# Optimization experiments

Hardware: AMD Instinct MI355X
Metric: run time of the kernel (lower is better)

## Reference

```python
import jax, jax.numpy as jnp
import numpy as np

U, I, E, D, R = 100000, 50000, 2000000, 64, 5


def setup_inputs() -> dict:
    key = jax.random.key(0)
    ks = jax.random.split(key, 14)
    def n(k, shape, scale=0.05):
        return jax.random.normal(k, shape, jnp.float32) * scale
    return {
        "user_feat": n(ks[0], (U, D), 1.0),
        "item_feat": n(ks[1], (I, D), 1.0),
        "rating_feat": n(ks[2], (R, D), 1.0),
        "row_idxs": jax.random.randint(ks[3], (E,), 0, I),   # item index per edge
        "col_idxs": jax.random.randint(ks[4], (E,), 0, U),   # user index per edge (dst)
        "rating": jax.random.randint(ks[5], (E,), 0, R),
        # gv = Linear(2D,D)+ReLU -> Linear(D,D)+ReLU
        "gv_w1": n(ks[6], (2 * D, D)), "gv_b1": jnp.zeros((D,), jnp.float32),
        "gv_w2": n(ks[7], (D, D)),     "gv_b2": jnp.zeros((D,), jnp.float32),
        # Attention: Linear(2D,D)+ReLU -> Linear(D,D)+ReLU -> Linear(D,1)
        "att_w1": n(ks[8], (2 * D, D)), "att_b1": jnp.zeros((D,), jnp.float32),
        "att_w2": n(ks[9], (D, D)),     "att_b2": jnp.zeros((D,), jnp.float32),
        "att_w3": n(ks[10], (D, 1)),    "att_b3": jnp.zeros((1,), jnp.float32),
        # output projection w = Linear(D,D)
        "w_w": n(ks[11], (D, D)), "w_b": jnp.zeros((D,), jnp.float32),
    }


def segment_softmax(logits, seg, num_segments):
    # numerically stable softmax over edges grouped by destination node
    m = jax.ops.segment_max(logits, seg, num_segments=num_segments)
    e = jnp.exp(logits - m[seg])
    s = jax.ops.segment_sum(e, seg, num_segments=num_segments)
    return e / s[seg]


def reference(user_feat, item_feat, rating_feat, row_idxs, col_idxs, rating,
              gv_w1, gv_b1, gv_w2, gv_b2,
              att_w1, att_b1, att_w2, att_b2, att_w3, att_b3,
              w_w, w_b):
    # gather per-edge embeddings
    r_emb = rating_feat[rating]          # [E, D]
    i_emb = item_feat[row_idxs]          # [E, D]
    u_emb = user_feat[col_idxs]          # [E, D]
    # gv MLP on concat(item, rating)
    x = jnp.concatenate([i_emb, r_emb], axis=1)              # [E, 2D]
    h1 = jax.nn.relu(x @ gv_w1 + gv_b1)
    x_ia = jax.nn.relu(h1 @ gv_w2 + gv_b2)                   # [E, D]
    # attention MLP on concat(x_ia, user)
    a = jnp.concatenate([x_ia, u_emb], axis=1)               # [E, 2D]
    a = jax.nn.relu(a @ att_w1 + att_b1)
    a = jax.nn.relu(a @ att_w2 + att_b2)
    weight = (a @ att_w3 + att_b3)[:, 0]                     # [E]
    # edge_softmax over incoming edges of each destination (user) node
    value = segment_softmax(weight, col_idxs, U)             # [E]
    # scatter-sum weighted messages to users
    h = jax.ops.segment_sum(x_ia * value[:, None], col_idxs, num_segments=U)  # [U, D]
    # act is None -> plain linear
    return h @ w_w + w_b
```

## Files before the change

### kernel.cpp

```cpp
#include <hip/hip_runtime.h>
#include <hip/hip_bf16.h>
#include <hip/hip_fp8.h>

#define U_N 100000
#define I_N 50000
#define E_N 2000000
#define R_N 5
#define C_N (I_N*R_N)
#define NBLK_E 7813
#define NBLK_C 1954
#define NBUCKC 196

typedef __hip_bfloat16 bf16_t;
typedef unsigned short u16;
typedef unsigned char u8;
typedef __attribute__((ext_vector_type(8))) short bf16x8;
typedef __attribute__((ext_vector_type(4))) float f32x4;

__device__ __forceinline__ float blo(unsigned u){ return __uint_as_float(u<<16); }
__device__ __forceinline__ float bhi(unsigned u){ return __uint_as_float(u & 0xffff0000u); }
__device__ __forceinline__ unsigned pkbf(float a, float b){
  __hip_bfloat162 t = __float22bfloat162_rn(float2{a,b});
  union { __hip_bfloat162 h; unsigned u; } cv; cv.h = t; return cv.u;
}
__device__ __forceinline__ u16 f2b(float v){
  union { __hip_bfloat16 h; u16 u; } cv; cv.h = __float2bfloat16(v); return cv.u;
}
__device__ __forceinline__ unsigned ff8(float f){
  __hip_fp8_e4m3 h(f); return (unsigned)h.__x;
}
__device__ __forceinline__ float2 f8x2(u16 h){
  __hip_fp8x2_e4m3 v; v.__x = h; return (float2)v;
}

__global__ __launch_bounds__(256) void k_histQ(const int* __restrict__ cols, int* __restrict__ hist_g){
  __shared__ int histI[NBUCKC];
  int t = threadIdx.x, b = blockIdx.x;
  if(t < NBUCKC) histI[t] = 0;
  __syncthreads();
  int e = b*256 + t;
  if(e < E_N) atomicAdd(&histI[cols[e] >> 9], 1);
  __syncthreads();
  if(t < NBUCKC) hist_g[(size_t)b*NBUCKC + t] = histI[t];
}

__global__ __launch_bounds__(256) void k_scanQ(const int* __restrict__ hist_g, int* __restrict__ boff_g,
                                               int* __restrict__ qtot){
  __shared__ int wsum[4];
  int t = threadIdx.x, q = blockIdx.x;
  int lane = t & 63, wv = t >> 6;
  int running = 0;
  for(int c0=0; c0<NBLK_E; c0+=256){
    int b = c0 + t;
    int v = (b < NBLK_E) ? hist_g[(size_t)b*NBUCKC + q] : 0;
    int inc = v;
#pragma unroll
    for(int off=1; off<64; off<<=1){
      int x = __shfl(inc, lane-off);
      if(lane >= off) inc += x;
    }
    if(lane == 63) wsum[wv] = inc;
    __syncthreads();
    int w0=wsum[0], w1=wsum[1], w2=wsum[2], w3=wsum[3];
    int wpre = (wv>0?w0:0) + (wv>1?w1:0) + (wv>2?w2:0);
    if(b < NBLK_E) boff_g[(size_t)b*NBUCKC + q] = running + wpre + inc - v;
    running += w0 + w1 + w2 + w3;
    __syncthreads();
  }
  if(t == 0) qtot[q] = running;
}

__global__ void k_scanT(const int* __restrict__ qtot, int* __restrict__ qbase){
  __shared__ int s[256];
  int t = threadIdx.x;
  int v = (t < NBUCKC) ? qtot[t] : 0;
  s[t] = v; __syncthreads();
  for(int off=1; off<256; off<<=1){
    int x = (t>=off) ? s[t-off] : 0;
    __syncthreads();
    s[t] += x;
    __syncthreads();
  }
  if(t < NBUCKC) qbase[t] = s[t] - v;
  if(t == 255)   qbase[NBUCKC] = s[255];
}

__global__ __launch_bounds__(256) void k_blockq(const int* __restrict__ qbase, int* __restrict__ blockq){
  int b = blockIdx.x*256 + threadIdx.x; if(b >= NBLK_E) return;
  int e = b*256;
  int lo = 0, hi = NBUCKC-1;
  while(lo < hi){ int mid = (lo+hi+1)>>1; if(qbase[mid] <= e) lo = mid; else hi = mid-1; }
  blockq[b] = lo;
}

__global__ __launch_bounds__(256) void k_place2(const int* __restrict__ rows, const int* __restrict__ cols,
                                                const int* __restrict__ rats,
                                                const int* __restrict__ boff_g, const int* __restrict__ qbase,
                                                unsigned* __restrict__ uc2){
  __shared__ int rankI[NBUCKC];
  __shared__ int baseI[NBUCKC];
  int t = threadIdx.x, b = blockIdx.x;
  if(t < NBUCKC){
    rankI[t] = 0;
    baseI[t] = qbase[t] + boff_g[(size_t)b*NBUCKC + t];
  }
  __syncthreads();
  int e = b*256 + t;
  if(e < E_N){
    int u = cols[e];
    int c = rows[e]*5 + rats[e];
    int q = u >> 9;
    int r = atomicAdd(&rankI[q], 1);
    uc2[baseI[q] + r] = ((unsigned)(u & 16383) << 18) | (unsigned)c;
  }
}

__global__ __launch_bounds__(256) void k_fine(const unsigned* __restrict__ uc2, const int* __restrict__ qbase,
                                              unsigned* __restrict__ uc3, int* __restrict__ start){
  __shared__ int histv[512];
  __shared__ int s[512];
  __shared__ int fillb[512];
  int t = threadIdx.x, q = blockIdx.x;
  histv[t]=0; histv[t+256]=0; fillb[t]=0; fillb[t+256]=0;
  __syncthreads();
  int r0 = qbase[q], r1 = qbase[q+1];
  for(int j=r0+t; j<r1; j+=256) atomicAdd(&histv[(uc2[j]>>18)&511], 1);
  __syncthreads();
  s[t]=histv[t]; s[t+256]=histv[t+256];
  __syncthreads();
  for(int off=1; off<512; off<<=1){
    int a0 = (t>=off)? s[t-off] : 0;
    int a1 = (t+256>=off)? s[t+256-off] : 0;
    __syncthreads();
    s[t]+=a0; s[t+256]+=a1;
    __syncthreads();
  }
  int e0 = s[t]-histv[t], e1 = s[t+256]-histv[t+256];
  start[q*512+t]     = r0 + e0;
  start[q*512+t+256] = r0 + e1;
  s[t]=e0; s[t+256]=e1;
  __syncthreads();
  for(int j=r0+t; j<r1; j+=256){
    unsigned v = uc2[j];
    int ul = (int)((v>>18)&511);
    int off = atomicAdd(&fillb[ul], 1);
    uc3[r0 + s[ul] + off] = v;
  }
}

__global__ void k_ratpart(const float* __restrict__ rf, const float* __restrict__ w1,
                          const float* __restrict__ b1, float* __restrict__ out){
  int t = threadIdx.x; if(t >= R_N*64) return;
  int r = t>>6, d = t&63;
  float acc = b1[d];
  for(int k=0;k<64;k++) acc += rf[r*64 + k] * w1[(64+k)*64 + d];
  out[t] = acc;
}

__global__ __launch_bounds__(256) void k_prepw6(const float* __restrict__ w1, const float* __restrict__ a1,
                                                const float* __restrict__ w2, const float* __restrict__ a2,
                                                const float* __restrict__ ww,
                                                u16* w1t, u16* u1t, u16* w2t, u16* a1t, u16* a2t, u16* wwt){
  int idx = (blockIdx.x & 15)*256 + threadIdx.x;
  int sec = blockIdx.x >> 4;
  int d = idx >> 6, k = idx & 63;
  const float* src; u16* dst; int ko = 0;
  switch(sec){
    case 0: src=w1; dst=w1t; break;
    case 1: src=a1; dst=u1t; ko=64; break;
    case 2: src=w2; dst=w2t; break;
    case 3: src=a1; dst=a1t; break;
    case 4: src=a2; dst=a2t; break;
    default: src=ww; dst=wwt; break;
  }
  dst[idx] = f2b(src[(size_t)(ko+k)*64 + d]);
}

template<bool BIAS>
__global__ __launch_bounds__(256) void k_rowgemm(const float4* __restrict__ in,
                                                 const uint4* __restrict__ wt,
                                                 const float* __restrict__ bias,
                                                 uint4* __restrict__ outp, int n){
  __shared__ uint4 A_u4[2048];
  __shared__ uint4 W_u4[512];
  __shared__ float bsh[64];
  u16* A16 = (u16*)A_u4;
  const int tid = threadIdx.x;
  for(int cid = tid; cid < 512; cid += 256){
    int dd = cid >> 3, ch = cid & 7;
    W_u4[dd*8 + (ch ^ (dd&7))] = wt[cid];
  }
  if(BIAS && tid < 64) bsh[tid] = bias[tid];
  const int base = blockIdx.x*256;
  const int ch = tid & 7;
#pragma unroll
  for(int it=0; it<8; ++it){
    int s = it*32 + (tid>>3);
    int r = base + s;
    uint4 o = {0,0,0,0};
    if(r < n){
      const float4* p = in + (size_t)r*16 + ch*2;
      float4 v0 = p[0], v1 = p[1];
      o.x = pkbf(v0.x, v0.y); o.y = pkbf(v0.z, v0.w);
      o.z = pkbf(v1.x, v1.y); o.w = pkbf(v1.z, v1.w);
    }
    A_u4[s*8 + (ch ^ (s&7))] = o;
  }
  __syncthreads();
  const int l = tid & 63, w = tid >> 6;
  const int lr = l & 15, g = l >> 4;
  bf16x8 bfr[4][2];
#pragma unroll
  for(int nt=0; nt<4; ++nt)
#pragma unroll
    for(int kk=0; kk<2; ++kk){
      int d = nt*16 + lr;
      bfr[nt][kk] = *(const bf16x8*)&W_u4[d*8 + ((kk*4+g) ^ (d&7))];
    }
  float bv[4];
#pragma unroll
  for(int nt=0; nt<4; ++nt) bv[nt] = BIAS ? bsh[nt*16 + lr] : 0.f;
#pragma unroll
  for(int t=0; t<4; ++t){
    int s = w*64 + t*16 + lr;
    bf16x8 af0 = *(const bf16x8*)&A_u4[s*8 + ((0*4+g) ^ (s&7))];
    bf16x8 af1 = *(const bf16x8*)&A_u4[s*8 + ((1*4+g) ^ (s&7))];
    f32x4 acc[4];
#pragma unroll
    for(int nt=0; nt<4; ++nt){
      f32x4 c0 = { bv[nt], bv[nt], bv[nt], bv[nt] };
      c0 = __builtin_amdgcn_mfma_f32_16x16x32_bf16(af0, bfr[nt][0], c0, 0, 0, 0);
      c0 = __builtin_amdgcn_mfma_f32_16x16x32_bf16(af1, bfr[nt][1], c0, 0, 0, 0);
      acc[nt] = c0;
    }
#pragma unroll
    for(int nt=0; nt<4; ++nt){
      int d = nt*16 + lr;
#pragma unroll
      for(int reg=0; reg<4; ++reg){
        int srow = w*64 + t*16 + g*4 + reg;
        A16[srow*64 + ((d>>3)^(srow&7))*8 + (d&7)] = f2b(acc[nt][reg]);
      }
    }
  }
#pragma unroll
  for(int it=0; it<8; ++it){
    int s = w*64 + it*8 + (l>>3);
    int c2 = l & 7;
    int r = base + s;
    if(r < n) outp[(size_t)r*8 + c2] = A_u4[s*8 + (c2 ^ (s&7))];
  }
}

__global__ __launch_bounds__(256) void k_combo_mfma(const uint4* __restrict__ itemp,
                                                    const float4* __restrict__ ratp,
                                                    const uint4* __restrict__ w2t_g, const uint4* __restrict__ a1t_g,
                                                    const uint4* __restrict__ wwt_g,
                                                    const float* __restrict__ b2,
                                                    uint4* __restrict__ y_o, u8* __restrict__ xa1_o8){
  __shared__ uint4 A_u4[1024];
  __shared__ uint4 X_u4[1024];
  __shared__ uint4 W2_u4[512];
  __shared__ uint4 A1_u4[512];
  __shared__ uint4 WW_u4[512];
  __shared__ float4 rsh4[80];
  __shared__ float b2sh[64];
  u16* A16 = (u16*)A_u4;
  u16* X16 = (u16*)X_u4;
  const int tid = threadIdx.x;
  for(int cid = tid; cid < 512; cid += 256){
    int dd = cid >> 3, ch = cid & 7;
    W2_u4[dd*8 + (ch ^ (dd&7))] = w2t_g[cid];
    A1_u4[dd*8 + (ch ^ (dd&7))] = a1t_g[cid];
    WW_u4[dd*8 + (ch ^ (dd&7))] = wwt_g[cid];
  }
  if(tid < 80) rsh4[tid] = ratp[tid];
  if(tid < 64) b2sh[tid] = b2[tid];
  __syncthreads();

  const int base = blockIdx.x*128;
  const int ch = tid & 7;
#pragma unroll
  for(int it=0; it<4; ++it){
    int s = it*32 + (tid>>3);
    int cidx = base + s;
    uint4 o = {0,0,0,0};
    if(cidx < C_N){
      int i = cidx/5, r = cidx - i*5;
      uint4 iv = itemp[(size_t)i*8 + ch];
      float4 r0 = rsh4[r*16 + ch*2], r1 = rsh4[r*16 + ch*2 + 1];
      o.x = pkbf(fmaxf(blo(iv.x)+r0.x,0.f), fmaxf(bhi(iv.x)+r0.y,0.f));
      o.y = pkbf(fmaxf(blo(iv.y)+r0.z,0.f), fmaxf(bhi(iv.y)+r0.w,0.f));
      o.z = pkbf(fmaxf(blo(iv.z)+r1.x,0.f), fmaxf(bhi(iv.z)+r1.y,0.f));
      o.w = pkbf(fmaxf(blo(iv.w)+r1.z,0.f), fmaxf(bhi(iv.w)+r1.w,0.f));
    }
    A_u4[s*8 + (ch ^ (s&7))] = o;
  }
  __syncthreads();

  const int l = tid & 63, w = tid >> 6;
  const int lr = l & 15, g = l >> 4;
  bf16x8 w2f[4][2], a1f[4][2], wwf[4][2];
#pragma unroll
  for(int nt=0; nt<4; ++nt)
#pragma unroll
    for(int kk=0; kk<2; ++kk){
      int d = nt*16 + lr;
      w2f[nt][kk] = *(const bf16x8*)&W2_u4[d*8 + ((kk*4+g) ^ (d&7))];
      a1f[nt][kk] = *(const bf16x8*)&A1_u4[d*8 + ((kk*4+g) ^ (d&7))];
      wwf[nt][kk] = *(const bf16x8*)&WW_u4[d*8 + ((kk*4+g) ^ (d&7))];
    }
  float b2v[4];
#pragma unroll
  for(int nt=0; nt<4; ++nt) b2v[nt] = b2sh[nt*16 + lr];

#pragma unroll
  for(int t=0; t<2; ++t){
    int s = w*32 + t*16 + lr;
    bf16x8 af0 = *(const bf16x8*)&A_u4[s*8 + ((0*4+g) ^ (s&7))];
    bf16x8 af1 = *(const bf16x8*)&A_u4[s*8 + ((1*4+g) ^ (s&7))];
#pragma unroll
    for(int nt=0; nt<4; ++nt){
      f32x4 c0 = { b2v[nt], b2v[nt], b2v[nt], b2v[nt] };
      c0 = __builtin_amdgcn_mfma_f32_16x16x32_bf16(af0, w2f[nt][0], c0, 0, 0, 0);
      c0 = __builtin_amdgcn_mfma_f32_16x16x32_bf16(af1, w2f[nt][1], c0, 0, 0, 0);
      int d = nt*16 + lr;
#pragma unroll
      for(int reg=0; reg<4; ++reg){
        int srow = w*32 + t*16 + g*4 + reg;
        X16[srow*64 + ((d>>3)^(srow&7))*8 + (d&7)] = f2b(fmaxf(c0[reg], 0.f));
      }
    }
    bf16x8 xf0 = *(const bf16x8*)&X_u4[s*8 + ((0*4+g) ^ (s&7))];
    bf16x8 xf1 = *(const bf16x8*)&X_u4[s*8 + ((1*4+g) ^ (s&7))];
#pragma unroll
    for(int nt=0; nt<4; ++nt){
      f32x4 c0 = { 0.f, 0.f, 0.f, 0.f };
      c0 = __builtin_amdgcn_mfma_f32_16x16x32_bf16(xf0, a1f[nt][0], c0, 0, 0, 0);
      c0 = __builtin_amdgcn_mfma_f32_16x16x32_bf16(xf1, a1f[nt][1], c0, 0, 0, 0);
      int d = nt*16 + lr;
#pragma unroll
      for(int reg=0; reg<4; ++reg){
        int srow = w*32 + t*16 + g*4 + reg;
        A16[srow*64 + ((d>>3)^(srow&7))*8 + (d&7)] = f2b(c0[reg]);
      }
    }
#pragma unroll
    for(int nt=0; nt<4; ++nt){
      f32x4 c0 = { 0.f, 0.f, 0.f, 0.f };
      c0 = __builtin_amdgcn_mfma_f32_16x16x32_bf16(xf0, wwf[nt][0], c0, 0, 0, 0);
      c0 = __builtin_amdgcn_mfma_f32_16x16x32_bf16(xf1, wwf[nt][1], c0, 0, 0, 0);
      int d = nt*16 + lr;
#pragma unroll
      for(int reg=0; reg<4; ++reg){
        int srow = w*32 + t*16 + g*4 + reg;
        X16[srow*64 + ((d>>3)^(srow&7))*8 + (d&7)] = f2b(c0[reg]);
      }
    }
  }
#pragma unroll
  for(int it=0; it<4; ++it){
    int s = w*32 + it*8 + (l>>3);
    int c2 = l & 7;
    int r = base + s;
    if(r < C_N) y_o[(size_t)r*8 + c2] = X_u4[s*8 + (c2 ^ (s&7))];
  }
#pragma unroll
  for(int it=0; it<2; ++it){
    int slot = it*64 + l;
    int rl = slot >> 2;
    int c4 = slot & 3;
    int s = w*32 + rl;
    int r = base + s;
    if(r < C_N){
      uint4 h0 = A_u4[s*8 + ((c4*2+0) ^ (s&7))];
      uint4 h1 = A_u4[s*8 + ((c4*2+1) ^ (s&7))];
      uint4 o;
      o.x = ff8(blo(h0.x)) | (ff8(bhi(h0.x))<<8) | (ff8(blo(h0.y))<<16) | (ff8(bhi(h0.y))<<24);
      o.y = ff8(blo(h0.z)) | (ff8(bhi(h0.z))<<8) | (ff8(blo(h0.w))<<16) | (ff8(bhi(h0.w))<<24);
      o.z = ff8(blo(h1.x)) | (ff8(bhi(h1.x))<<8) | (ff8(blo(h1.y))<<16) | (ff8(bhi(h1.y))<<24);
      o.w = ff8(blo(h1.z)) | (ff8(bhi(h1.z))<<8) | (ff8(blo(h1.w))<<16) | (ff8(bhi(h1.w))<<24);
      *(uint4*)(xa1_o8 + (size_t)r*64 + c4*16) = o;
    }
  }
}

__global__ __launch_bounds__(256) void k_edge_mfma(const unsigned* __restrict__ uc3,
                                                   const int* __restrict__ qbase, const int* __restrict__ blockq,
                                                   const u8* __restrict__ xa1p8, const uint4* __restrict__ userp,
                                                   const u16* __restrict__ w2t_g,
                                                   const float* __restrict__ a2b,
                                                   const float* __restrict__ a3w, const float* __restrict__ a3b,
                                                   float* __restrict__ wlog){
  const int tid = threadIdx.x;
  const int base = blockIdx.x*256;
  const int l = tid & 63, w = tid >> 6;
  const int lr = l & 15;
  const int g  = l >> 4;
  bf16x8 bf[4][2];
#pragma unroll
  for(int nt=0; nt<4; ++nt)
#pragma unroll
    for(int kk=0; kk<2; ++kk){
      int d = nt*16 + lr;
      bf[nt][kk] = *(const bf16x8*)(w2t_g + d*64 + kk*32 + g*8);
    }
  float b2v[4], a3v[4];
#pragma unroll
  for(int nt=0; nt<4; ++nt){ b2v[nt] = a2b[nt*16 + lr]; a3v[nt] = a3w[nt*16 + lr]; }
  const float a3b0 = a3b[0];

  int cin[4], uin[4];
  int bq = blockq[blockIdx.x];
#pragma unroll
  for(int t=0; t<4; ++t){
    int s = base + w*64 + t*16 + lr;
    int sc = (s < E_N) ? s : (E_N-1);
    unsigned vv = (s < E_N) ? uc3[s] : 0u;
    int q = bq;
    while(sc >= qbase[q+1]) ++q;
    cin[t] = (int)(vv & 0x3FFFFu);
    uin[t] = (q<<9) | (int)((vv>>18) & 511u);
  }

  auto compute = [&](uint2 xq0, uint2 xq1, uint4 uv0, uint4 uv1, int t){
    union { uint4 u4; bf16x8 v; } a0, a1;
    {
      float2 p01 = f8x2((u16)xq0.x), p23 = f8x2((u16)(xq0.x>>16));
      float2 p45 = f8x2((u16)xq0.y), p67 = f8x2((u16)(xq0.y>>16));
      a0.u4.x = pkbf(fmaxf(p01.x+blo(uv0.x),0.f), fmaxf(p01.y+bhi(uv0.x),0.f));
      a0.u4.y = pkbf(fmaxf(p23.x+blo(uv0.y),0.f), fmaxf(p23.y+bhi(uv0.y),0.f));
      a0.u4.z = pkbf(fmaxf(p45.x+blo(uv0.z),0.f), fmaxf(p45.y+bhi(uv0.z),0.f));
      a0.u4.w = pkbf(fmaxf(p67.x+blo(uv0.w),0.f), fmaxf(p67.y+bhi(uv0.w),0.f));
      p01 = f8x2((u16)xq1.x); p23 = f8x2((u16)(xq1.x>>16));
      p45 = f8x2((u16)xq1.y); p67 = f8x2((u16)(xq1.y>>16));
      a1.u4.x = pkbf(fmaxf(p01.x+blo(uv1.x),0.f), fmaxf(p01.y+bhi(uv1.x),0.f));
      a1.u4.y = pkbf(fmaxf(p23.x+blo(uv1.y),0.f), fmaxf(p23.y+bhi(uv1.y),0.f));
      a1.u4.z = pkbf(fmaxf(p45.x+blo(uv1.z),0.f), fmaxf(p45.y+bhi(uv1.z),0.f));
      a1.u4.w = pkbf(fmaxf(p67.x+blo(uv1.w),0.f), fmaxf(p67.y+bhi(uv1.w),0.f));
    }
    f32x4 acc[4];
#pragma unroll
    for(int nt=0; nt<4; ++nt){
      f32x4 c0 = { b2v[nt], b2v[nt], b2v[nt], b2v[nt] };
      c0 = __builtin_amdgcn_mfma_f32_16x16x32_bf16(a0.v, bf[nt][0], c0, 0, 0, 0);
      c0 = __builtin_amdgcn_mfma_f32_16x16x32_bf16(a1.v, bf[nt][1], c0, 0, 0, 0);
      acc[nt] = c0;
    }
    float s0=0.f, s1=0.f, s2=0.f, s3=0.f;
#pragma unroll
    for(int nt=0; nt<4; ++nt){
      s0 += fmaxf(acc[nt][0], 0.f) * a3v[nt];
      s1 += fmaxf(acc[nt][1], 0.f) * a3v[nt];
      s2 += fmaxf(acc[nt][2], 0.f) * a3v[nt];
      s3 += fmaxf(acc[nt][3], 0.f) * a3v[nt];
    }
#pragma unroll
    for(int mask=1; mask<16; mask<<=1){
      s0 += __shfl_xor(s0, mask);
      s1 += __shfl_xor(s1, mask);
      s2 += __shfl_xor(s2, mask);
      s3 += __shfl_xor(s3, mask);
    }
    if(lr == 0){
      int e0 = base + w*64 + t*16 + g*4;
      if(e0+0 < E_N) wlog[e0+0] = s0 + a3b0;
      if(e0+1 < E_N) wlog[e0+1] = s1 + a3b0;
      if(e0+2 < E_N) wlog[e0+2] = s2 + a3b0;
      if(e0+3 < E_N) wlog[e0+3] = s3 + a3b0;
    }
  };

  uint2 xA0 = *(const uint2*)(xa1p8 + (size_t)cin[0]*64 + g*8);
  uint2 xA1 = *(const uint2*)(xa1p8 + (size_t)cin[0]*64 + 32 + g*8);
  uint4 uA0 = userp[(size_t)uin[0]*8 + g];
  uint4 uA1 = userp[(size_t)uin[0]*8 + 4 + g];
  uint2 xB0 = *(const uint2*)(xa1p8 + (size_t)cin[1]*64 + g*8);
  uint2 xB1 = *(const uint2*)(xa1p8 + (size_t)cin[1]*64 + 32 + g*8);
  uint4 uB0 = userp[(size_t)uin[1]*8 + g];
  uint4 uB1 = userp[(size_t)uin[1]*8 + 4 + g];

  compute(xA0, xA1, uA0, uA1, 0);
  xA0 = *(const uint2*)(xa1p8 + (size_t)cin[2]*64 + g*8);
  xA1 = *(const uint2*)(xa1p8 + (size_t)cin[2]*64 + 32 + g*8);
  uA0 = userp[(size_t)uin[2]*8 + g];
  uA1 = userp[(size_t)uin[2]*8 + 4 + g];
  compute(xB0, xB1, uB0, uB1, 1);
  xB0 = *(const uint2*)(xa1p8 + (size_t)cin[3]*64 + g*8);
  xB1 = *(const uint2*)(xa1p8 + (size_t)cin[3]*64 + 32 + g*8);
  uB0 = userp[(size_t)uin[3]*8 + g];
  uB1 = userp[(size_t)uin[3]*8 + 4 + g];
  compute(xA0, xA1, uA0, uA1, 2);
  compute(xB0, xB1, uB0, uB1, 3);
}

__global__ __launch_bounds__(256) void k_aggf(const int* __restrict__ start,
                                              const unsigned* __restrict__ uc3,
                                              const float* __restrict__ wlog,
                                              const u16* __restrict__ Y,
                                              const float* __restrict__ wb,
                                              float* __restrict__ out){
  __shared__ uint4 Ysh[2][4][256];
  int w = threadIdx.x >> 6, l = threadIdx.x & 63;
  int lr = l & 15, g = l >> 4;
  int base = (blockIdx.x*4 + w) * 16;
  if(base >= U_N) return;
  int s0g = start[base];
  int s1g = start[base+16];
  unsigned ml = (unsigned)((base + lr) & 16383);
  int sA = s0g & ~31;
  int nch = (s1g - sA + 31) >> 5;
  const int kb = g*8;

  f32x4 acc[4];
#pragma unroll
  for(int nt=0; nt<4; ++nt) acc[nt] = f32x4{0.f,0.f,0.f,0.f};
  float ssum = 0.f;
  int buf = 0;
  if(nch > 0){
    int rowe = sA + (l>>1);
    int crow = (int)(uc3[rowe] & 0x3FFFFu);
    const uint4* yp = (const uint4*)Y + (size_t)crow*8 + (l&1)*4;
    uint4 y0=yp[0], y1=yp[1], y2=yp[2], y3=yp[3];
    uint4* dst = &Ysh[0][w][(l>>1)*8 + (l&1)*4];
    dst[0]=y0; dst[1]=y1; dst[2]=y2; dst[3]=y3;
  }
  for(int ch=0; ch<nch; ++ch){
    int e0 = sA + ch*32;
    uint4 n0, n1, n2, n3;
    bool hasNext = (ch+1 < nch);
    if(hasNext){
      int rowe = e0 + 32 + (l>>1);
      int crowN = (int)(uc3[rowe] & 0x3FFFFu);
      const uint4* yp = (const uint4*)Y + (size_t)crowN*8 + (l&1)*4;
      n0=yp[0]; n1=yp[1]; n2=yp[2]; n3=yp[3];
    }
    float4 wv0 = *(const float4*)(wlog + e0 + kb);
    float4 wv1 = *(const float4*)(wlog + e0 + kb + 4);
    uint4 v0 = *(const uint4*)(uc3 + e0 + kb);
    uint4 v1 = *(const uint4*)(uc3 + e0 + kb + 4);
    bf16x8 af;
    {
      bool mt; float e;
      mt = ((v0.x>>18)==ml); e = __expf(mt?wv0.x:-1e30f); ssum += e; af[0] = mt?(short)f2b(e):(short)0;
      mt = ((v0.y>>18)==ml); e = __expf(mt?wv0.y:-1e30f); ssum += e; af[1] = mt?(short)f2b(e):(short)0;
      mt = ((v0.z>>18)==ml); e = __expf(mt?wv0.z:-1e30f); ssum += e; af[2] = mt?(short)f2b(e):(short)0;
      mt = ((v0.w>>18)==ml); e = __expf(mt?wv0.w:-1e30f); ssum += e; af[3] = mt?(short)f2b(e):(short)0;
      mt = ((v1.x>>18)==ml); e = __expf(mt?wv1.x:-1e30f); ssum += e; af[4] = mt?(short)f2b(e):(short)0;
      mt = ((v1.y>>18)==ml); e = __expf(mt?wv1.y:-1e30f); ssum += e; af[5] = mt?(short)f2b(e):(short)0;
      mt = ((v1.z>>18)==ml); e = __expf(mt?wv1.z:-1e30f); ssum += e; af[6] = mt?(short)f2b(e):(short)0;
      mt = ((v1.w>>18)==ml); e = __expf(mt?wv1.w:-1e30f); ssum += e; af[7] = mt?(short)f2b(e):(short)0;
    }
    u16* Ysh16 = (u16*)&Ysh[buf][w][0];
    bf16x8 b0, b1, b2, b3;
#pragma unroll
    for(int j=0; j<8; ++j){
      int r = (kb + j)*64 + lr;
      b0[j] = (short)Ysh16[r];
      b1[j] = (short)Ysh16[r+16];
      b2[j] = (short)Ysh16[r+32];
      b3[j] = (short)Ysh16[r+48];
    }
    acc[0] = __builtin_amdgcn_mfma_f32_16x16x32_bf16(af, b0, acc[0], 0, 0, 0);
    acc[1] = __builtin_amdgcn_mfma_f32_16x16x32_bf16(af, b1, acc[1], 0, 0, 0);
    acc[2] = __builtin_amdgcn_mfma_f32_16x16x32_bf16(af, b2, acc[2], 0, 0, 0);
    acc[3] = __builtin_amdgcn_mfma_f32_16x16x32_bf16(af, b3, acc[3], 0, 0, 0);
    if(hasNext){
      uint4* dst = &Ysh[buf^1][w][(l>>1)*8 + (l&1)*4];
      dst[0]=n0; dst[1]=n1; dst[2]=n2; dst[3]=n3;
    }
    buf ^= 1;
  }
  ssum += __shfl_xor(ssum, 16);
  ssum += __shfl_xor(ssum, 32);
  float inv = (ssum > 0.f) ? (1.f/ssum) : 0.f;
  float wbv[4];
#pragma unroll
  for(int nt=0; nt<4; ++nt) wbv[nt] = wb[nt*16 + lr];
#pragma unroll
  for(int reg=0; reg<4; ++reg){
    float sc = __shfl(inv, g*4 + reg);
    int u = base + g*4 + reg;
#pragma unroll
    for(int nt=0; nt<4; ++nt)
      out[(size_t)u*64 + nt*16 + lr] = acc[nt][reg]*sc + wbv[nt];
  }
}

extern "C" void kernel_launch(void* const* d_in, const int* in_sizes, int n_in,
                              void* d_out, int out_size, void* d_ws, size_t ws_size,
                              hipStream_t stream){
  (void)in_sizes; (void)n_in; (void)out_size; (void)ws_size;
  const float4* user_feat  = (const float4*)d_in[0];
  const float4* item_feat  = (const float4*)d_in[1];
  const float*  rating_feat= (const float*)d_in[2];
  const int*    rows       = (const int*)d_in[3];
  const int*    cols       = (const int*)d_in[4];
  const int*    rats       = (const int*)d_in[5];
  const float* gv_w1 = (const float*)d_in[6];
  const float* gv_b1 = (const float*)d_in[7];
  const float* gv_w2 = (const float*)d_in[8];
  const float* gv_b2 = (const float*)d_in[9];
  const float* att_w1= (const float*)d_in[10];
  const float* att_b1= (const float*)d_in[11];
  const float* att_w2= (const float*)d_in[12];
  const float* att_b2= (const float*)d_in[13];
  const float* att_w3= (const float*)d_in[14];
  const float* att_b3= (const float*)d_in[15];
  const float* w_w   = (const float*)d_in[16];
  const float* w_b   = (const float*)d_in[17];
  float* out = (float*)d_out;

  char* ws = (char*)d_ws; size_t off = 0;
  auto take = [&](size_t b)->char*{ char* p = ws + off; off = (off + b + 255) & ~(size_t)255; return p; };
  bf16_t*   item_part  = (bf16_t*)take((size_t)I_N*64*2);
  bf16_t*   user_part  = (bf16_t*)take((size_t)U_N*64*2);
  float*    rating_part= (float*) take((size_t)R_N*64*4);
  bf16_t*   y_t        = (bf16_t*)take((size_t)C_N*64*2);
  u8*       xa1_8      = (u8*)    take((size_t)C_N*64);
  float*    wlog_s     = (float*) take((size_t)E_N*4);
  unsigned* uc3        = (unsigned*)take((size_t)E_N*4);
  unsigned* uc2        = (unsigned*)take((size_t)E_N*4);
  int*      hist_g     = (int*)   take((size_t)NBLK_E*NBUCKC*4);
  int*      boff_g     = (int*)   take((size_t)NBLK_E*NBUCKC*4);
  int*      qtot       = (int*)   take((size_t)256*4);
  int*      qbase      = (int*)   take((size_t)256*4);
  int*      blockq     = (int*)   take((size_t)NBLK_E*4);
  int*      start      = (int*)   take((size_t)(NBUCKC*512+64)*4);
  u16*      w1t        = (u16*)   take((size_t)4096*2);
  u16*      u1t        = (u16*)   take((size_t)4096*2);
  u16*      w2t        = (u16*)   take((size_t)4096*2);
  u16*      a1t        = (u16*)   take((size_t)4096*2);
  u16*      a2t        = (u16*)   take((size_t)4096*2);
  u16*      wwt        = (u16*)   take((size_t)4096*2);

  k_histQ <<<NBLK_E, 256, 0, stream>>>(cols, hist_g);
  k_scanQ <<<NBUCKC, 256, 0, stream>>>(hist_g, boff_g, qtot);
  k_scanT <<<1, 256, 0, stream>>>(qtot, qbase);
  k_blockq<<<(NBLK_E+255)/256, 256, 0, stream>>>(qbase, blockq);
  k_place2<<<NBLK_E, 256, 0, stream>>>(rows, cols, rats, boff_g, qbase, uc2);
  k_fine  <<<NBUCKC, 256, 0, stream>>>(uc2, qbase, uc3, start);
  k_ratpart <<<1, 320, 0, stream>>>(rating_feat, gv_w1, gv_b1, rating_part);
  k_prepw6  <<<96, 256, 0, stream>>>(gv_w1, att_w1, gv_w2, att_w2, w_w, w1t, u1t, w2t, a1t, a2t, wwt);
  k_rowgemm<false><<<(I_N+255)/256, 256, 0, stream>>>(item_feat, (const uint4*)w1t, nullptr,
                                                      (uint4*)item_part, I_N);
  k_rowgemm<true> <<<(U_N+255)/256, 256, 0, stream>>>(user_feat, (const uint4*)u1t, att_b1,
                                                      (uint4*)user_part, U_N);
  k_combo_mfma<<<NBLK_C, 256, 0, stream>>>((const uint4*)item_part, (const float4*)rating_part,
                                           (const uint4*)w2t, (const uint4*)a1t, (const uint4*)wwt, gv_b2,
                                           (uint4*)y_t, xa1_8);
  k_edge_mfma<<<NBLK_E, 256, 0, stream>>>(uc3, qbase, blockq, xa1_8, (const uint4*)user_part,
                                          w2t, att_b2, att_w3, att_b3, wlog_s);
  k_aggf <<<(U_N/64)+1, 256, 0, stream>>>(start, uc3, wlog_s, (const u16*)y_t, w_b, out);
}
```

Before: 263.8 us.

## Fuse edge attention MLP into per-user aggregation kernel

Merges the per-edge attention MLP kernel and the aggregation kernel into one kernel that works per group of 16 destination users. Each wave computes attention logits for its 32-edge chunk, exponentiates them into shared memory and uses them directly as softmax weights. The user rows come from a shared-memory tile, so the wlog buffer round trip, the blockq kernel and the per-edge user gathers all go away. In exchange, edges in chunks that straddle user-group boundaries are computed more than once, the Y double-buffer prefetch is removed, and the max subtraction is dropped from the softmax (it was already absent before).

Measured after the change: 277.8 us. 5.3% more time.

```diff
diff --git a/kernel.cpp b/kernel.cpp
--- a/kernel.cpp
+++ b/kernel.cpp
@@ -83,14 +83,6 @@
   }
   if(t < NBUCKC) qbase[t] = s[t] - v;
   if(t == 255)   qbase[NBUCKC] = s[255];
-}
-
-__global__ __launch_bounds__(256) void k_blockq(const int* __restrict__ qbase, int* __restrict__ blockq){
-  int b = blockIdx.x*256 + threadIdx.x; if(b >= NBLK_E) return;
-  int e = b*256;
-  int lo = 0, hi = NBUCKC-1;
-  while(lo < hi){ int mid = (lo+hi+1)>>1; if(qbase[mid] <= e) lo = mid; else hi = mid-1; }
-  blockq[b] = lo;
 }
 
 __global__ __launch_bounds__(256) void k_place2(const int* __restrict__ rows, const int* __restrict__ cols,
@@ -385,18 +377,25 @@
   }
 }
 
-__global__ __launch_bounds__(256) void k_edge_mfma(const unsigned* __restrict__ uc3,
-                                                   const int* __restrict__ qbase, const int* __restrict__ blockq,
-                                                   const u8* __restrict__ xa1p8, const uint4* __restrict__ userp,
-                                                   const u16* __restrict__ w2t_g,
-                                                   const float* __restrict__ a2b,
-                                                   const float* __restrict__ a3w, const float* __restrict__ a3b,
-                                                   float* __restrict__ wlog){
+__global__ __launch_bounds__(256) void k_fused(const int* __restrict__ start,
+                                               const unsigned* __restrict__ uc3,
+                                               const u8* __restrict__ xa1p8,
+                                               const uint4* __restrict__ userp,
+                                               const u16* __restrict__ w2t_g,
+                                               const float* __restrict__ a2b,
+                                               const float* __restrict__ a3w, const float* __restrict__ a3b,
+                                               const u16* __restrict__ Y,
+                                               const float* __restrict__ wb,
+                                               float* __restrict__ out){
+  __shared__ uint4 Ush[4][16][8];
+  __shared__ uint4 Ysh[4][256];
+  __shared__ float pl[4][32];
   const int tid = threadIdx.x;
-  const int base = blockIdx.x*256;
-  const int l = tid & 63, w = tid >> 6;
-  const int lr = l & 15;
-  const int g  = l >> 4;
+  int w = tid >> 6, l = tid & 63;
+  int lr = l & 15, g = l >> 4;
+  int base = (blockIdx.x*4 + w) * 16;
+  if(base >= U_N) return;
+
   bf16x8 bf[4][2];
 #pragma unroll
   for(int nt=0; nt<4; ++nt)
@@ -410,104 +409,15 @@
   for(int nt=0; nt<4; ++nt){ b2v[nt] = a2b[nt*16 + lr]; a3v[nt] = a3w[nt*16 + lr]; }
   const float a3b0 = a3b[0];
 
-  int cin[4], uin[4];
-  int bq = blockq[blockIdx.x];
-#pragma unroll
-  for(int t=0; t<4; ++t){
-    int s = base + w*64 + t*16 + lr;
-    int sc = (s < E_N) ? s : (E_N-1);
-    unsigned vv = (s < E_N) ? uc3[s] : 0u;
-    int q = bq;
-    while(sc >= qbase[q+1]) ++q;
-    cin[t] = (int)(vv & 0x3FFFFu);
-    uin[t] = (q<<9) | (int)((vv>>18) & 511u);
-  }
-
-  auto compute = [&](uint2 xq0, uint2 xq1, uint4 uv0, uint4 uv1, int t){
-    union { uint4 u4; bf16x8 v; } a0, a1;
-    {
-      float2 p01 = f8x2((u16)xq0.x), p23 = f8x2((u16)(xq0.x>>16));
-      float2 p45 = f8x2((u16)xq0.y), p67 = f8x2((u16)(xq0.y>>16));
-      a0.u4.x = pkbf(fmaxf(p01.x+blo(uv0.x),0.f), fmaxf(p01.y+bhi(uv0.x),0.f));
-      a0.u4.y = pkbf(fmaxf(p23.x+blo(uv0.y),0.f), fmaxf(p23.y+bhi(uv0.y),0.f));
-      a0.u4.z = pkbf(fmaxf(p45.x+blo(uv0.z),0.f), fmaxf(p45.y+bhi(uv0.z),0.f));
-      a0.u4.w = pkbf(fmaxf(p67.x+blo(uv0.w),0.f), fmaxf(p67.y+bhi(uv0.w),0.f));
-      p01 = f8x2((u16)xq1.x); p23 = f8x2((u16)(xq1.x>>16));
-      p45 = f8x2((u16)xq1.y); p67 = f8x2((u16)(xq1.y>>16));
-      a1.u4.x = pkbf(fmaxf(p01.x+blo(uv1.x),0.f), fmaxf(p01.y+bhi(uv1.x),0.f));
-      a1.u4.y = pkbf(fmaxf(p23.x+blo(uv1.y),0.f), fmaxf(p23.y+bhi(uv1.y),0.f));
-      a1.u4.z = pkbf(fmaxf(p45.x+blo(uv1.z),0.f), fmaxf(p45.y+bhi(uv1.z),0.f));
-      a1.u4.w = pkbf(fmaxf(p67.x+blo(uv1.w),0.f), fmaxf(p67.y+bhi(uv1.w),0.f));
-    }
-    f32x4 acc[4];
-#pragma unroll
-    for(int nt=0; nt<4; ++nt){
-      f32x4 c0 = { b2v[nt], b2v[nt], b2v[nt], b2v[nt] };
-      c0 = __builtin_amdgcn_mfma_f32_16x16x32_bf16(a0.v, bf[nt][0], c0, 0, 0, 0);
-      c0 = __builtin_amdgcn_mfma_f32_16x16x32_bf16(a1.v, bf[nt][1], c0, 0, 0, 0);
-      acc[nt] = c0;
-    }
-    float s0=0.f, s1=0.f, s2=0.f, s3=0.f;
-#pragma unroll
-    for(int nt=0; nt<4; ++nt){
-      s0 += fmaxf(acc[nt][0], 0.f) * a3v[nt];
-      s1 += fmaxf(acc[nt][1], 0.f) * a3v[nt];
-      s2 += fmaxf(acc[nt][2], 0.f) * a3v[nt];
-      s3 += fmaxf(acc[nt][3], 0.f) * a3v[nt];
-    }
-#pragma unroll
-    for(int mask=1; mask<16; mask<<=1){
-      s0 += __shfl_xor(s0, mask);
-      s1 += __shfl_xor(s1, mask);
-      s2 += __shfl_xor(s2, mask);
-      s3 += __shfl_xor(s3, mask);
-    }
-    if(lr == 0){
-      int e0 = base + w*64 + t*16 + g*4;
-      if(e0+0 < E_N) wlog[e0+0] = s0 + a3b0;
-      if(e0+1 < E_N) wlog[e0+1] = s1 + a3b0;
-      if(e0+2 < E_N) wlog[e0+2] = s2 + a3b0;
-      if(e0+3 < E_N) wlog[e0+3] = s3 + a3b0;
-    }
-  };
-
-  uint2 xA0 = *(const uint2*)(xa1p8 + (size_t)cin[0]*64 + g*8);
-  uint2 xA1 = *(const uint2*)(xa1p8 + (size_t)cin[0]*64 + 32 + g*8);
-  uint4 uA0 = userp[(size_t)uin[0]*8 + g];
-  uint4 uA1 = userp[(size_t)uin[0]*8 + 4 + g];
-  uint2 xB0 = *(const uint2*)(xa1p8 + (size_t)cin[1]*64 + g*8);
-  uint2 xB1 = *(const uint2*)(xa1p8 + (size_t)cin[1]*64 + 32 + g*8);
-  uint4 uB0 = userp[(size_t)uin[1]*8 + g];
-  uint4 uB1 = userp[(size_t)uin[1]*8 + 4 + g];
-
-  compute(xA0, xA1, uA0, uA1, 0);
-  xA0 = *(const uint2*)(xa1p8 + (size_t)cin[2]*64 + g*8);
-  xA1 = *(const uint2*)(xa1p8 + (size_t)cin[2]*64 + 32 + g*8);
-  uA0 = userp[(size_t)uin[2]*8 + g];
-  uA1 = userp[(size_t)uin[2]*8 + 4 + g];
-  compute(xB0, xB1, uB0, uB1, 1);
-  xB0 = *(const uint2*)(xa1p8 + (size_t)cin[3]*64 + g*8);
-  xB1 = *(const uint2*)(xa1p8 + (size_t)cin[3]*64 + 32 + g*8);
-  uB0 = userp[(size_t)uin[3]*8 + g];
-  uB1 = userp[(size_t)uin[3]*8 + 4 + g];
-  compute(xA0, xA1, uA0, uA1, 2);
-  compute(xB0, xB1, uB0, uB1, 3);
-}
-
-__global__ __launch_bounds__(256) void k_aggf(const int* __restrict__ start,
-                                              const unsigned* __restrict__ uc3,
-                                              const float* __restrict__ wlog,
-                                              const u16* __restrict__ Y,
-                                              const float* __restrict__ wb,
-                                              float* __restrict__ out){
-  __shared__ uint4 Ysh[2][4][256];
-  int w = threadIdx.x >> 6, l = threadIdx.x & 63;
-  int lr = l & 15, g = l >> 4;
-  int base = (blockIdx.x*4 + w) * 16;
-  if(base >= U_N) return;
+  {
+    int idx0 = l*2;
+    int row = idx0 >> 3, col = idx0 & 7;
+    Ush[w][row][col]   = userp[(size_t)(base+row)*8 + col];
+    Ush[w][row][col+1] = userp[(size_t)(base+row)*8 + col+1];
+  }
+
   int s0g = start[base];
   int s1g = start[base+16];
-  unsigned ml = (unsigned)((base + lr) & 16383);
   int sA = s0g & ~31;
   int nch = (s1g - sA + 31) >> 5;
   const int kb = g*8;
@@ -516,42 +426,89 @@
 #pragma unroll
   for(int nt=0; nt<4; ++nt) acc[nt] = f32x4{0.f,0.f,0.f,0.f};
   float ssum = 0.f;
-  int buf = 0;
-  if(nch > 0){
-    int rowe = sA + (l>>1);
+
+  for(int ch=0; ch<nch; ++ch){
+    int e0 = sA + ch*32;
+    int rowe = e0 + (l>>1);
     int crow = (int)(uc3[rowe] & 0x3FFFFu);
     const uint4* yp = (const uint4*)Y + (size_t)crow*8 + (l&1)*4;
     uint4 y0=yp[0], y1=yp[1], y2=yp[2], y3=yp[3];
-    uint4* dst = &Ysh[0][w][(l>>1)*8 + (l&1)*4];
-    dst[0]=y0; dst[1]=y1; dst[2]=y2; dst[3]=y3;
-  }
-  for(int ch=0; ch<nch; ++ch){
-    int e0 = sA + ch*32;
-    uint4 n0, n1, n2, n3;
-    bool hasNext = (ch+1 < nch);
-    if(hasNext){
-      int rowe = e0 + 32 + (l>>1);
-      int crowN = (int)(uc3[rowe] & 0x3FFFFu);
-      const uint4* yp = (const uint4*)Y + (size_t)crowN*8 + (l&1)*4;
-      n0=yp[0]; n1=yp[1]; n2=yp[2]; n3=yp[3];
-    }
-    float4 wv0 = *(const float4*)(wlog + e0 + kb);
-    float4 wv1 = *(const float4*)(wlog + e0 + kb + 4);
+
+#pragma unroll
+    for(int t=0; t<2; ++t){
+      int et = e0 + t*16 + lr;
+      unsigned v = uc3[et];
+      int c = (int)(v & 0x3FFFFu);
+      unsigned ul = ((v>>18) - (unsigned)base) & 16383u;
+      int ulc = (ul < 16u) ? (int)ul : 0;
+      uint2 xq0 = *(const uint2*)(xa1p8 + (size_t)c*64 + g*8);
+      uint2 xq1 = *(const uint2*)(xa1p8 + (size_t)c*64 + 32 + g*8);
+      uint4 uv0 = Ush[w][ulc][g];
+      uint4 uv1 = Ush[w][ulc][4+g];
+      union { uint4 u4; bf16x8 v8; } a0, a1;
+      {
+        float2 p01 = f8x2((u16)xq0.x), p23 = f8x2((u16)(xq0.x>>16));
+        float2 p45 = f8x2((u16)xq0.y), p67 = f8x2((u16)(xq0.y>>16));
+        a0.u4.x = pkbf(fmaxf(p01.x+blo(uv0.x),0.f), fmaxf(p01.y+bhi(uv0.x),0.f));
+        a0.u4.y = pkbf(fmaxf(p23.x+blo(uv0.y),0.f), fmaxf(p23.y+bhi(uv0.y),0.f));
+        a0.u4.z = pkbf(fmaxf(p45.x+blo(uv0.z),0.f), fmaxf(p45.y+bhi(uv0.z),0.f));
+        a0.u4.w = pkbf(fmaxf(p67.x+blo(uv0.w),0.f), fmaxf(p67.y+bhi(uv0.w),0.f));
+        p01 = f8x2((u16)xq1.x); p23 = f8x2((u16)(xq1.x>>16));
+        p45 = f8x2((u16)xq1.y); p67 = f8x2((u16)(xq1.y>>16));
+        a1.u4.x = pkbf(fmaxf(p01.x+blo(uv1.x),0.f), fmaxf(p01.y+bhi(uv1.x),0.f));
+        a1.u4.y = pkbf(fmaxf(p23.x+blo(uv1.y),0.f), fmaxf(p23.y+bhi(uv1.y),0.f));
+        a1.u4.z = pkbf(fmaxf(p45.x+blo(uv1.z),0.f), fmaxf(p45.y+bhi(uv1.z),0.f));
+        a1.u4.w = pkbf(fmaxf(p67.x+blo(uv1.w),0.f), fmaxf(p67.y+bhi(uv1.w),0.f));
+      }
+      f32x4 acc2[4];
+#pragma unroll
+      for(int nt=0; nt<4; ++nt){
+        f32x4 c0 = { b2v[nt], b2v[nt], b2v[nt], b2v[nt] };
+        c0 = __builtin_amdgcn_mfma_f32_16x16x32_bf16(a0.v8, bf[nt][0], c0, 0, 0, 0);
+        c0 = __builtin_amdgcn_mfma_f32_16x16x32_bf16(a1.v8, bf[nt][1], c0, 0, 0, 0);
+        acc2[nt] = c0;
+      }
+      float s0=0.f, s1=0.f, s2=0.f, s3=0.f;
+#pragma unroll
+      for(int nt=0; nt<4; ++nt){
+        s0 += fmaxf(acc2[nt][0], 0.f) * a3v[nt];
+        s1 += fmaxf(acc2[nt][1], 0.f) * a3v[nt];
+        s2 += fmaxf(acc2[nt][2], 0.f) * a3v[nt];
+        s3 += fmaxf(acc2[nt][3], 0.f) * a3v[nt];
+      }
+#pragma unroll
+      for(int mask=1; mask<16; mask<<=1){
+        s0 += __shfl_xor(s0, mask);
+        s1 += __shfl_xor(s1, mask);
+        s2 += __shfl_xor(s2, mask);
+        s3 += __shfl_xor(s3, mask);
+      }
+      if(lr == 0){
+        pl[w][t*16 + g*4 + 0] = __expf(s0 + a3b0);
+        pl[w][t*16 + g*4 + 1] = __expf(s1 + a3b0);
+        pl[w][t*16 + g*4 + 2] = __expf(s2 + a3b0);
+        pl[w][t*16 + g*4 + 3] = __expf(s3 + a3b0);
+      }
+    }
+    {
+      uint4* dst = &Ysh[w][(l>>1)*8 + (l&1)*4];
+      dst[0]=y0; dst[1]=y1; dst[2]=y2; dst[3]=y3;
+    }
     uint4 v0 = *(const uint4*)(uc3 + e0 + kb);
     uint4 v1 = *(const uint4*)(uc3 + e0 + kb + 4);
     bf16x8 af;
     {
-      bool mt; float e;
-      mt = ((v0.x>>18)==ml); e = __expf(mt?wv0.x:-1e30f); ssum += e; af[0] = mt?(short)f2b(e):(short)0;
-      mt = ((v0.y>>18)==ml); e = __expf(mt?wv0.y:-1e30f); ssum += e; af[1] = mt?(short)f2b(e):(short)0;
-      mt = ((v0.z>>18)==ml); e = __expf(mt?wv0.z:-1e30f); ssum += e; af[2] = mt?(short)f2b(e):(short)0;
-      mt = ((v0.w>>18)==ml); e = __expf(mt?wv0.w:-1e30f); ssum += e; af[3] = mt?(short)f2b(e):(short)0;
-      mt = ((v1.x>>18)==ml); e = __expf(mt?wv1.x:-1e30f); ssum += e; af[4] = mt?(short)f2b(e):(short)0;
-      mt = ((v1.y>>18)==ml); e = __expf(mt?wv1.y:-1e30f); ssum += e; af[5] = mt?(short)f2b(e):(short)0;
-      mt = ((v1.z>>18)==ml); e = __expf(mt?wv1.z:-1e30f); ssum += e; af[6] = mt?(short)f2b(e):(short)0;
-      mt = ((v1.w>>18)==ml); e = __expf(mt?wv1.w:-1e30f); ssum += e; af[7] = mt?(short)f2b(e):(short)0;
-    }
-    u16* Ysh16 = (u16*)&Ysh[buf][w][0];
+      float pv; bool mt;
+      mt = ((((v0.x>>18) - (unsigned)base) & 16383u) == (unsigned)lr); pv = pl[w][kb+0]; ssum += mt?pv:0.f; af[0] = mt?(short)f2b(pv):(short)0;
+      mt = ((((v0.y>>18) - (unsigned)base) & 16383u) == (unsigned)lr); pv = pl[w][kb+1]; ssum += mt?pv:0.f; af[1] = mt?(short)f2b(pv):(short)0;
+      mt = ((((v0.z>>18) - (unsigned)base) & 16383u) == (unsigned)lr); pv = pl[w][kb+2]; ssum += mt?pv:0.f; af[2] = mt?(short)f2b(pv):(short)0;
+      mt = ((((v0.w>>18) - (unsigned)base) & 16383u) == (unsigned)lr); pv = pl[w][kb+3]; ssum += mt?pv:0.f; af[3] = mt?(short)f2b(pv):(short)0;
+      mt = ((((v1.x>>18) - (unsigned)base) & 16383u) == (unsigned)lr); pv = pl[w][kb+4]; ssum += mt?pv:0.f; af[4] = mt?(short)f2b(pv):(short)0;
+      mt = ((((v1.y>>18) - (unsigned)base) & 16383u) == (unsigned)lr); pv = pl[w][kb+5]; ssum += mt?pv:0.f; af[5] = mt?(short)f2b(pv):(short)0;
+      mt = ((((v1.z>>18) - (unsigned)base) & 16383u) == (unsigned)lr); pv = pl[w][kb+6]; ssum += mt?pv:0.f; af[6] = mt?(short)f2b(pv):(short)0;
+      mt = ((((v1.w>>18) - (unsigned)base) & 16383u) == (unsigned)lr); pv = pl[w][kb+7]; ssum += mt?pv:0.f; af[7] = mt?(short)f2b(pv):(short)0;
+    }
+    u16* Ysh16 = (u16*)&Ysh[w][0];
     bf16x8 b0, b1, b2, b3;
 #pragma unroll
     for(int j=0; j<8; ++j){
@@ -565,11 +522,6 @@
     acc[1] = __builtin_amdgcn_mfma_f32_16x16x32_bf16(af, b1, acc[1], 0, 0, 0);
     acc[2] = __builtin_amdgcn_mfma_f32_16x16x32_bf16(af, b2, acc[2], 0, 0, 0);
     acc[3] = __builtin_amdgcn_mfma_f32_16x16x32_bf16(af, b3, acc[3], 0, 0, 0);
-    if(hasNext){
-      uint4* dst = &Ysh[buf^1][w][(l>>1)*8 + (l&1)*4];
-      dst[0]=n0; dst[1]=n1; dst[2]=n2; dst[3]=n3;
-    }
-    buf ^= 1;
   }
   ssum += __shfl_xor(ssum, 16);
   ssum += __shfl_xor(ssum, 32);
@@ -618,14 +570,12 @@
   float*    rating_part= (float*) take((size_t)R_N*64*4);
   bf16_t*   y_t        = (bf16_t*)take((size_t)C_N*64*2);
   u8*       xa1_8      = (u8*)    take((size_t)C_N*64);
-  float*    wlog_s     = (float*) take((size_t)E_N*4);
   unsigned* uc3        = (unsigned*)take((size_t)E_N*4);
   unsigned* uc2        = (unsigned*)take((size_t)E_N*4);
   int*      hist_g     = (int*)   take((size_t)NBLK_E*NBUCKC*4);
   int*      boff_g     = (int*)   take((size_t)NBLK_E*NBUCKC*4);
   int*      qtot       = (int*)   take((size_t)256*4);
   int*      qbase      = (int*)   take((size_t)256*4);
-  int*      blockq     = (int*)   take((size_t)NBLK_E*4);
   int*      start      = (int*)   take((size_t)(NBUCKC*512+64)*4);
   u16*      w1t        = (u16*)   take((size_t)4096*2);
   u16*      u1t        = (u16*)   take((size_t)4096*2);
@@ -637,7 +587,6 @@
   k_histQ <<<NBLK_E, 256, 0, stream>>>(cols, hist_g);
   k_scanQ <<<NBUCKC, 256, 0, stream>>>(hist_g, boff_g, qtot);
   k_scanT <<<1, 256, 0, stream>>>(qtot, qbase);
-  k_blockq<<<(NBLK_E+255)/256, 256, 0, stream>>>(qbase, blockq);
   k_place2<<<NBLK_E, 256, 0, stream>>>(rows, cols, rats, boff_g, qbase, uc2);
   k_fine  <<<NBUCKC, 256, 0, stream>>>(uc2, qbase, uc3, start);
   k_ratpart <<<1, 320, 0, stream>>>(rating_feat, gv_w1, gv_b1, rating_part);
@@ -649,7 +598,7 @@
   k_combo_mfma<<<NBLK_C, 256, 0, stream>>>((const uint4*)item_part, (const float4*)rating_part,
                                            (const uint4*)w2t, (const uint4*)a1t, (const uint4*)wwt, gv_b2,
                                            (uint4*)y_t, xa1_8);
-  k_edge_mfma<<<NBLK_E, 256, 0, stream>>>(uc3, qbase, blockq, xa1_8, (const uint4*)user_part,
-                                          w2t, att_b2, att_w3, att_b3, wlog_s);
-  k_aggf <<<(U_N/64)+1, 256, 0, stream>>>(start, uc3, wlog_s, (const u16*)y_t, w_b, out);
-}
+  k_fused<<<(U_N/64)+1, 256, 0, stream>>>(start, uc3, xa1_8, (const uint4*)user_part,
+                                          w2t, att_b2, att_w3, att_b3,
+                                          (const u16*)y_t, w_b, out);
+}
```
